# Kernel tuning notes

Hardware: AMD Instinct MI355X
Metric: run time of the kernel (lower is better)

## Reference

```python
import jax, jax.numpy as jnp
import numpy as np

B, N, D = 2, 2048, 768
HEADS, DIM_HEAD = 12, 64
INNER = HEADS * DIM_HEAD  # 768
OUT_DIM = 768


def setup_inputs() -> dict:
    key = jax.random.key(0)
    k1, k2, k3, k4, k5 = jax.random.split(key, 5)
    s_in = 1.0 / np.sqrt(D)
    s_inner = 1.0 / np.sqrt(INNER)
    return {
        "x": jax.random.normal(k1, (B, N, D), dtype=jnp.float32),
        "w_qkv": jax.random.normal(k2, (D, 3 * INNER), dtype=jnp.float32) * s_in,
        "b_qkv": jax.random.normal(k3, (3 * INNER,), dtype=jnp.float32) * 0.01,
        "w_out": jax.random.normal(k4, (INNER, OUT_DIM), dtype=jnp.float32) * s_inner,
        "b_out": jax.random.normal(k5, (OUT_DIM,), dtype=jnp.float32) * 0.01,
    }


def reference(x, w_qkv, b_qkv, w_out, b_out):
    b, n, _ = x.shape
    scale = DIM_HEAD ** -0.5
    qkv = x @ w_qkv + b_qkv                      # [b, n, 3*inner]
    q, k, v = jnp.split(qkv, 3, axis=-1)
    # 'b n (h d) -> b h n d'
    reshape = lambda t: t.reshape(b, n, HEADS, DIM_HEAD).transpose(0, 2, 1, 3)
    q, k, v = reshape(q), reshape(k), reshape(v)
    dots = jnp.einsum("bhnd,bhmd->bhnm", q, k) * scale
    attn = jax.nn.softmax(dots, axis=-1)
    out = jnp.einsum("bhnm,bhmd->bhnd", attn, v)  # [b, h, n, d]
    out = out.transpose(0, 2, 1, 3).reshape(b, n, INNER)
    return out @ w_out + b_out
```

## Files before the change

kernel.cpp:

```cpp
#include <hip/hip_runtime.h>
#include <hip/hip_bf16.h>
#include <stdint.h>


typedef __attribute__((ext_vector_type(8))) short bf16x8;
typedef __attribute__((ext_vector_type(4))) float f32x4;
typedef __attribute__((address_space(3))) unsigned int lds_uint;
typedef __attribute__((address_space(1))) const unsigned int g_uint;

__device__ __forceinline__ short f2bf(float f) {
    union { float f; uint32_t u; } x; x.f = f;
    uint32_t r = (x.u + 0x7fffu + ((x.u >> 16) & 1u)) >> 16;
    return (short)r;
}
__device__ __forceinline__ float exp2fast(float x) {
#if __has_builtin(__builtin_amdgcn_exp2f)
    return __builtin_amdgcn_exp2f(x);
#else
    return __expf(x * 0.6931471805599453f);
#endif
}
__device__ __forceinline__ void gl_lds16(const void* g, void* l) {
    __builtin_amdgcn_global_load_lds((g_uint*)g, (lds_uint*)l, 16, 0, 0);
}

__device__ __forceinline__ void tr_tile(const float* __restrict__ W,
                                        short* __restrict__ Wt, int K, int N,
                                        int n0, int k0, int t, short* S) {
    {
        int kl = t >> 2, ng = t & 3;
        const float* src = W + (size_t)(k0 + kl) * N + n0 + ng * 16;
        #pragma unroll
        for (int j = 0; j < 16; j += 4) {
            float4 f = *(const float4*)(src + j);
            S[(ng*16 + j + 0) * 65 + kl] = f2bf(f.x);
            S[(ng*16 + j + 1) * 65 + kl] = f2bf(f.y);
            S[(ng*16 + j + 2) * 65 + kl] = f2bf(f.z);
            S[(ng*16 + j + 3) * 65 + kl] = f2bf(f.w);
        }
    }
    __syncthreads();
    {
        int nl = t >> 2, kg = t & 3;
        short* dst = Wt + (size_t)(n0 + nl) * K + k0 + kg * 16;
        #pragma unroll
        for (int j = 0; j < 16; j += 4) {
            short4 s4;
            s4.x = S[nl*65 + kg*16 + j + 0];
            s4.y = S[nl*65 + kg*16 + j + 1];
            s4.z = S[nl*65 + kg*16 + j + 2];
            s4.w = S[nl*65 + kg*16 + j + 3];
            *(short4*)(dst + j) = s4;
        }
    }
}

__global__ __launch_bounds__(256)
void prep_k(const float* __restrict__ x, short* __restrict__ Xb,
            const float* __restrict__ Wq, short* __restrict__ Wqt,
            const float* __restrict__ Wo, short* __restrict__ Wot)
{
    __shared__ short S[64 * 65];
    const int t = threadIdx.x;
    if (blockIdx.x < 1536) {
        int i = (blockIdx.x * 256 + t) * 8;
        float4 f0 = *(const float4*)(x + i);
        float4 f1 = *(const float4*)(x + i + 4);
        short s[8];
        s[0]=f2bf(f0.x); s[1]=f2bf(f0.y); s[2]=f2bf(f0.z); s[3]=f2bf(f0.w);
        s[4]=f2bf(f1.x); s[5]=f2bf(f1.y); s[6]=f2bf(f1.z); s[7]=f2bf(f1.w);
        *(uint4*)(Xb + i) = *(uint4*)s;
        return;
    }
    if (blockIdx.x < 1968) {
        const int b2 = blockIdx.x - 1536;
        tr_tile(Wq, Wqt, 768, 2304, (b2 % 36) * 64, (b2 / 36) * 64, t, S);
    } else {
        const int b3 = blockIdx.x - 1968;
        tr_tile(Wo, Wot, 768, 768, (b3 % 12) * 64, (b3 / 12) * 64, t, S);
    }
}

__global__ __launch_bounds__(256)
void tr_w(const float* __restrict__ W, short* __restrict__ Wt, int K, int N) {
    __shared__ short S[64 * 65];
    tr_tile(W, Wt, K, N, blockIdx.x * 64, blockIdx.y * 64, threadIdx.x, S);
}

__global__ __launch_bounds__(256)
void gemm_qkv(const short* __restrict__ A, const short* __restrict__ Bt,
              const float* __restrict__ bias,
              short* __restrict__ Qb, short* __restrict__ Kb, short* __restrict__ Vt)
{
    __shared__ short As[128 * 32];
    __shared__ short Bs[128 * 32];
    const int tid = threadIdx.x, lane = tid & 63, w = tid >> 6;
    const int wm = w >> 1, wn = w & 1, quad = lane >> 4, lcol = lane & 15;
    const int bm = blockIdx.y * 128, bn = blockIdx.x * 128;

    f32x4 acc[4][4];
    #pragma unroll
    for (int i = 0; i < 4; i++)
        #pragma unroll
        for (int j = 0; j < 4; j++) acc[i][j] = (f32x4){0.f, 0.f, 0.f, 0.f};

    for (int kt = 0; kt < 768; kt += 32) {
        #pragma unroll
        for (int i = 0; i < 2; i++) {
            int c = tid + i * 256, row = c >> 2, cs = c & 3;
            gl_lds16(A  + (size_t)(bm + row) * 768 + kt + cs * 8, As + c * 8);
        }
        #pragma unroll
        for (int i = 0; i < 2; i++) {
            int c = tid + i * 256, row = c >> 2, cs = c & 3;
            gl_lds16(Bt + (size_t)(bn + row) * 768 + kt + cs * 8, Bs + c * 8);
        }
        __syncthreads();
        bf16x8 a[4], b[4];
        #pragma unroll
        for (int tm = 0; tm < 4; tm++)
            a[tm] = *(const bf16x8*)(As + (wm*64 + tm*16 + lcol) * 32 + quad * 8);
        #pragma unroll
        for (int tn = 0; tn < 4; tn++)
            b[tn] = *(const bf16x8*)(Bs + (wn*64 + tn*16 + lcol) * 32 + quad * 8);
        #pragma unroll
        for (int tm = 0; tm < 4; tm++)
            #pragma unroll
            for (int tn = 0; tn < 4; tn++)
                acc[tm][tn] = __builtin_amdgcn_mfma_f32_16x16x32_bf16(a[tm], b[tn], acc[tm][tn], 0, 0, 0);
        __syncthreads();
    }

    const float SCLQ = 0.18033688011112042f;
    #pragma unroll
    for (int tm = 0; tm < 4; tm++) {
        #pragma unroll
        for (int tn = 0; tn < 4; tn++) {
            int col = bn + wn*64 + tn*16 + lcol;
            float bv = bias[col];
            int which = (col >= 1536) ? 2 : (col >= 768 ? 1 : 0);
            int cc = col - which * 768;
            int h = cc >> 6, d = cc & 63;
            int rowbase = bm + wm*64 + tm*16 + quad*4;
            int bb = rowbase >> 11, n0 = rowbase & 2047;
            int bh = bb * 12 + h;
            if (which == 2) {
                short4 s4;
                s4.x = f2bf(acc[tm][tn][0] + bv);
                s4.y = f2bf(acc[tm][tn][1] + bv);
                s4.z = f2bf(acc[tm][tn][2] + bv);
                s4.w = f2bf(acc[tm][tn][3] + bv);
                *(short4*)(Vt + (((size_t)bh*32 + (n0 >> 6))*64 + d)*64 + (n0 & 63)) = s4;
            } else {
                #pragma unroll
                for (int reg = 0; reg < 4; reg++) {
                    float v = acc[tm][tn][reg] + bv;
                    if (which == 0) v *= SCLQ;
                    short* dst = (which == 0) ? Qb : Kb;
                    dst[((size_t)bh*2048 + n0 + reg)*64 + d] = f2bf(v);
                }
            }
        }
    }
}

__global__ __launch_bounds__(256)
void attn_k(const short* __restrict__ Q, const short* __restrict__ K,
            const short* __restrict__ Vt, short* __restrict__ Ab)
{
    __shared__ short Ks[2][4096];
    __shared__ short Vs[2][4096];
    __shared__ short Ps[4][16 * 72];

    const int tid = threadIdx.x, lane = tid & 63, w = tid >> 6;
    const int quad = lane >> 4, lcol = lane & 15;
    const int bid = blockIdx.x;
    const int bh = bid % 24, qt = bid / 24;
    const int b = bh / 12, h = bh - b * 12;

    const short* Kg = K  + (size_t)bh * 131072;
    const short* Vg = Vt + (size_t)bh * 131072;

    bf16x8 qf[2];
    {
        const short* Qg = Q + ((size_t)bh * 2048 + (size_t)qt * 64 + w * 16 + lcol) * 64;
        qf[0] = *(const bf16x8*)(Qg + quad * 8);
        qf[1] = *(const bf16x8*)(Qg + 32 + quad * 8);
    }

    #pragma unroll
    for (int i = 0; i < 2; i++) {
        int c = tid + i * 256, row = c >> 3, cs = c & 7, gc = cs ^ (row & 7);
        gl_lds16(Kg + row * 64 + gc * 8, Ks[0] + c * 8);
        gl_lds16(Vg + row * 64 + gc * 8, Vs[0] + c * 8);
    }
    __syncthreads();

    f32x4 o[4];
    #pragma unroll
    for (int tn = 0; tn < 4; tn++) o[tn] = (f32x4){0.f, 0.f, 0.f, 0.f};
    float lp[4] = {0.f, 0.f, 0.f, 0.f};

    short* Pw = Ps[w];

    for (int kt = 0; kt < 32; kt++) {
        const int p = kt & 1;
        if (kt < 31) {
            #pragma unroll
            for (int i = 0; i < 2; i++) {
                int c = tid + i * 256, row = c >> 3, cs = c & 7, gc = cs ^ (row & 7);
                gl_lds16(Kg + (kt + 1) * 4096 + row * 64 + gc * 8, Ks[p ^ 1] + c * 8);
                gl_lds16(Vg + (kt + 1) * 4096 + row * 64 + gc * 8, Vs[p ^ 1] + c * 8);
            }
        }

        f32x4 st[4];
        #pragma unroll
        for (int tn = 0; tn < 4; tn++) st[tn] = (f32x4){0.f, 0.f, 0.f, 0.f};
        #pragma unroll
        for (int ks = 0; ks < 2; ks++) {
            #pragma unroll
            for (int tn = 0; tn < 4; tn++) {
                int row = tn * 16 + lcol;
                bf16x8 bk = *(const bf16x8*)(Ks[p] + row * 64 +
                                             (((ks * 4 + quad) ^ (row & 7)) << 3));
                st[tn] = __builtin_amdgcn_mfma_f32_16x16x32_bf16(qf[ks], bk, st[tn], 0, 0, 0);
            }
        }

        #pragma unroll
        for (int tn = 0; tn < 4; tn++) {
            #pragma unroll
            for (int r = 0; r < 4; r++) {
                float pv = exp2fast(st[tn][r]);
                lp[r] += pv;
                union { float f; uint32_t u; } c; c.f = pv;
                Pw[(quad*4 + r) * 72 + tn*16 + lcol] = (short)((c.u + 0x8000u) >> 16);
            }
        }

        #pragma unroll
        for (int ks = 0; ks < 2; ks++) {
            bf16x8 ap = *(const bf16x8*)(Pw + lcol * 72 + ks * 32 + quad * 8);
            #pragma unroll
            for (int tn = 0; tn < 4; tn++) {
                int row = tn * 16 + lcol;
                bf16x8 bv = *(const bf16x8*)(Vs[p] + row * 64 +
                                             (((ks * 4 + quad) ^ (row & 7)) << 3));
                o[tn] = __builtin_amdgcn_mfma_f32_16x16x32_bf16(ap, bv, o[tn], 0, 0, 0);
            }
        }
        __syncthreads();
    }

    float rl[4];
    #pragma unroll
    for (int r = 0; r < 4; r++) {
        float v = lp[r];
        v += __shfl_xor(v, 1, 16);
        v += __shfl_xor(v, 2, 16);
        v += __shfl_xor(v, 4, 16);
        v += __shfl_xor(v, 8, 16);
        rl[r] = 1.0f / v;
    }
    #pragma unroll
    for (int tn = 0; tn < 4; tn++) {
        #pragma unroll
        for (int r = 0; r < 4; r++) {
            int q = qt * 64 + w * 16 + quad * 4 + r;
            int d = h * 64 + tn * 16 + lcol;
            Ab[((size_t)(b * 2048 + q)) * 768 + d] = f2bf(o[tn][r] * rl[r]);
        }
    }
}

__global__ __launch_bounds__(256)
void gemm_out64(const short* __restrict__ A, const short* __restrict__ Bt,
                const float* __restrict__ bias, float* __restrict__ Of)
{
    __shared__ short As[64 * 32];
    __shared__ short Bs[64 * 32];
    const int tid = threadIdx.x, lane = tid & 63, w = tid >> 6;
    const int wm = w >> 1, wn = w & 1, quad = lane >> 4, lcol = lane & 15;
    const int bm = blockIdx.y * 64, bn = blockIdx.x * 64;

    f32x4 acc[2][2];
    #pragma unroll
    for (int i = 0; i < 2; i++)
        #pragma unroll
        for (int j = 0; j < 2; j++) acc[i][j] = (f32x4){0.f, 0.f, 0.f, 0.f};

    for (int kt = 0; kt < 768; kt += 32) {
        {
            int row = tid >> 2, cs = tid & 3;
            gl_lds16(A  + (size_t)(bm + row) * 768 + kt + cs * 8, As + tid * 8);
            gl_lds16(Bt + (size_t)(bn + row) * 768 + kt + cs * 8, Bs + tid * 8);
        }
        __syncthreads();
        bf16x8 a[2], b[2];
        #pragma unroll
        for (int tm = 0; tm < 2; tm++)
            a[tm] = *(const bf16x8*)(As + (wm*32 + tm*16 + lcol) * 32 + quad * 8);
        #pragma unroll
        for (int tn = 0; tn < 2; tn++)
            b[tn] = *(const bf16x8*)(Bs + (wn*32 + tn*16 + lcol) * 32 + quad * 8);
        #pragma unroll
        for (int tm = 0; tm < 2; tm++)
            #pragma unroll
            for (int tn = 0; tn < 2; tn++)
                acc[tm][tn] = __builtin_amdgcn_mfma_f32_16x16x32_bf16(a[tm], b[tn], acc[tm][tn], 0, 0, 0);
        __syncthreads();
    }
    #pragma unroll
    for (int tm = 0; tm < 2; tm++) {
        #pragma unroll
        for (int tn = 0; tn < 2; tn++) {
            int col = bn + wn*32 + tn*16 + lcol;
            float bv = bias[col];
            #pragma unroll
            for (int reg = 0; reg < 4; reg++) {
                int row = bm + wm*32 + tm*16 + quad*4 + reg;
                Of[(size_t)row * 768 + col] = acc[tm][tn][reg] + bv;
            }
        }
    }
}

extern "C" void kernel_launch(void* const* d_in, const int* in_sizes, int n_in,
                              void* d_out, int out_size, void* d_ws, size_t ws_size,
                              hipStream_t stream)
{
    (void)in_sizes; (void)n_in; (void)out_size;
    const float* x     = (const float*)d_in[0];
    const float* w_qkv = (const float*)d_in[1];
    const float* b_qkv = (const float*)d_in[2];
    const float* w_out = (const float*)d_in[3];
    const float* b_out = (const float*)d_in[4];
    float* out = (float*)d_out;

    const size_t XSZ = (size_t)4096 * 768;
    const size_t WQ  = (size_t)2304 * 768;
    const size_t WO  = (size_t)768 * 768;
    const size_t HSZ = (size_t)24 * 2048 * 64;
    short* Xb  = (short*)d_ws;
    short* Wqt = Xb + XSZ;
    short* Qb  = Wqt + WQ;
    short* Kb  = Qb + HSZ;
    short* Vt  = Kb + HSZ;
    short* Ab  = Xb;

    const bool sepWot = ws_size >= (XSZ + WQ + 3*HSZ + WO) * sizeof(short);
    short* Wot = sepWot ? (Vt + HSZ) : Wqt;

    if (sepWot) {
        prep_k<<<2112, 256, 0, stream>>>(x, Xb, w_qkv, Wqt, w_out, Wot);
        gemm_qkv<<<dim3(18, 32), 256, 0, stream>>>(Xb, Wqt, b_qkv, Qb, Kb, Vt);
    } else {
        prep_k<<<1968, 256, 0, stream>>>(x, Xb, w_qkv, Wqt, w_out, Wot);
        gemm_qkv<<<dim3(18, 32), 256, 0, stream>>>(Xb, Wqt, b_qkv, Qb, Kb, Vt);
        tr_w<<<dim3(12, 12), 256, 0, stream>>>(w_out, Wot, 768, 768);
    }
    attn_k<<<768, 256, 0, stream>>>(Qb, Kb, Vt, Ab);
    gemm_out64<<<dim3(12, 64), 256, 0, stream>>>(Ab, Wot, b_out, out);
}
```

Measured before the change: 181.5 us.

## Enlarge attention query tile to 128 rows and widen output GEMM tile

The attention kernel now runs 512 threads per block covering 128 query rows, so each K/V tile load to LDS is shared by twice as many queries. Each thread now issues one async load per tile instead of two. Bf16 packing of the probabilities uses the paired conversion intrinsic, and the P buffer row stride changes from 72 to 68. The output projection GEMM widens its N tile to 96 with a 2x3 MFMA layout per warp, which improves operand reuse. The cost is fewer blocks (384 attention, 512 GEMM), which lowers parallelism on a large-CU device, and possible LDS bank conflicts from the new stride.

Measured after the change: 203.4 us. 1.12x slower.

```diff
diff --git a/kernel.cpp b/kernel.cpp
--- a/kernel.cpp
+++ b/kernel.cpp
@@ -164,13 +164,13 @@
     }
 }
 
-__global__ __launch_bounds__(256)
+__global__ __launch_bounds__(512)
 void attn_k(const short* __restrict__ Q, const short* __restrict__ K,
             const short* __restrict__ Vt, short* __restrict__ Ab)
 {
     __shared__ short Ks[2][4096];
     __shared__ short Vs[2][4096];
-    __shared__ short Ps[4][16 * 72];
+    __shared__ short Ps[8][16 * 68];
 
     const int tid = threadIdx.x, lane = tid & 63, w = tid >> 6;
     const int quad = lane >> 4, lcol = lane & 15;
@@ -183,14 +183,13 @@
 
     bf16x8 qf[2];
     {
-        const short* Qg = Q + ((size_t)bh * 2048 + (size_t)qt * 64 + w * 16 + lcol) * 64;
+        const short* Qg = Q + ((size_t)bh * 2048 + (size_t)qt * 128 + w * 16 + lcol) * 64;
         qf[0] = *(const bf16x8*)(Qg + quad * 8);
         qf[1] = *(const bf16x8*)(Qg + 32 + quad * 8);
     }
 
-    #pragma unroll
-    for (int i = 0; i < 2; i++) {
-        int c = tid + i * 256, row = c >> 3, cs = c & 7, gc = cs ^ (row & 7);
+    {
+        int c = tid, row = c >> 3, cs = c & 7, gc = cs ^ (row & 7);
         gl_lds16(Kg + row * 64 + gc * 8, Ks[0] + c * 8);
         gl_lds16(Vg + row * 64 + gc * 8, Vs[0] + c * 8);
     }
@@ -206,12 +205,9 @@
     for (int kt = 0; kt < 32; kt++) {
         const int p = kt & 1;
         if (kt < 31) {
-            #pragma unroll
-            for (int i = 0; i < 2; i++) {
-                int c = tid + i * 256, row = c >> 3, cs = c & 7, gc = cs ^ (row & 7);
-                gl_lds16(Kg + (kt + 1) * 4096 + row * 64 + gc * 8, Ks[p ^ 1] + c * 8);
-                gl_lds16(Vg + (kt + 1) * 4096 + row * 64 + gc * 8, Vs[p ^ 1] + c * 8);
-            }
+            int c = tid, row = c >> 3, cs = c & 7, gc = cs ^ (row & 7);
+            gl_lds16(Kg + (kt + 1) * 4096 + row * 64 + gc * 8, Ks[p ^ 1] + c * 8);
+            gl_lds16(Vg + (kt + 1) * 4096 + row * 64 + gc * 8, Vs[p ^ 1] + c * 8);
         }
 
         f32x4 st[4];
@@ -230,18 +226,21 @@
 
         #pragma unroll
         for (int tn = 0; tn < 4; tn++) {
-            #pragma unroll
-            for (int r = 0; r < 4; r++) {
-                float pv = exp2fast(st[tn][r]);
-                lp[r] += pv;
-                union { float f; uint32_t u; } c; c.f = pv;
-                Pw[(quad*4 + r) * 72 + tn*16 + lcol] = (short)((c.u + 0x8000u) >> 16);
-            }
+            float p0 = exp2fast(st[tn][0]), p1 = exp2fast(st[tn][1]);
+            float p2 = exp2fast(st[tn][2]), p3 = exp2fast(st[tn][3]);
+            lp[0] += p0; lp[1] += p1; lp[2] += p2; lp[3] += p3;
+            union { __hip_bfloat162 h2; uint32_t u; short s[2]; } c01, c23;
+            c01.h2 = __float22bfloat162_rn(make_float2(p0, p1));
+            c23.h2 = __float22bfloat162_rn(make_float2(p2, p3));
+            Pw[(quad*4 + 0) * 68 + tn*16 + lcol] = c01.s[0];
+            Pw[(quad*4 + 1) * 68 + tn*16 + lcol] = c01.s[1];
+            Pw[(quad*4 + 2) * 68 + tn*16 + lcol] = c23.s[0];
+            Pw[(quad*4 + 3) * 68 + tn*16 + lcol] = c23.s[1];
         }
 
         #pragma unroll
         for (int ks = 0; ks < 2; ks++) {
-            bf16x8 ap = *(const bf16x8*)(Pw + lcol * 72 + ks * 32 + quad * 8);
+            bf16x8 ap = *(const bf16x8*)(Pw + lcol * 68 + ks * 32 + quad * 8);
             #pragma unroll
             for (int tn = 0; tn < 4; tn++) {
                 int row = tn * 16 + lcol;
@@ -267,7 +266,7 @@
     for (int tn = 0; tn < 4; tn++) {
         #pragma unroll
         for (int r = 0; r < 4; r++) {
-            int q = qt * 64 + w * 16 + quad * 4 + r;
+            int q = qt * 128 + w * 16 + quad * 4 + r;
             int d = h * 64 + tn * 16 + lcol;
             Ab[((size_t)(b * 2048 + q)) * 768 + d] = f2bf(o[tn][r] * rl[r]);
         }
@@ -275,20 +274,20 @@
 }
 
 __global__ __launch_bounds__(256)
-void gemm_out64(const short* __restrict__ A, const short* __restrict__ Bt,
-                const float* __restrict__ bias, float* __restrict__ Of)
+void gemm_out(const short* __restrict__ A, const short* __restrict__ Bt,
+              const float* __restrict__ bias, float* __restrict__ Of)
 {
     __shared__ short As[64 * 32];
-    __shared__ short Bs[64 * 32];
+    __shared__ short Bs[96 * 32];
     const int tid = threadIdx.x, lane = tid & 63, w = tid >> 6;
     const int wm = w >> 1, wn = w & 1, quad = lane >> 4, lcol = lane & 15;
-    const int bm = blockIdx.y * 64, bn = blockIdx.x * 64;
-
-    f32x4 acc[2][2];
+    const int bm = blockIdx.y * 64, bn = blockIdx.x * 96;
+
+    f32x4 acc[2][3];
     #pragma unroll
     for (int i = 0; i < 2; i++)
         #pragma unroll
-        for (int j = 0; j < 2; j++) acc[i][j] = (f32x4){0.f, 0.f, 0.f, 0.f};
+        for (int j = 0; j < 3; j++) acc[i][j] = (f32x4){0.f, 0.f, 0.f, 0.f};
 
     for (int kt = 0; kt < 768; kt += 32) {
         {
@@ -296,26 +295,30 @@
             gl_lds16(A  + (size_t)(bm + row) * 768 + kt + cs * 8, As + tid * 8);
             gl_lds16(Bt + (size_t)(bn + row) * 768 + kt + cs * 8, Bs + tid * 8);
         }
-        __syncthreads();
-        bf16x8 a[2], b[2];
+        if (tid < 128) {
+            int c = 256 + tid, row = c >> 2, cs = c & 3;
+            gl_lds16(Bt + (size_t)(bn + row) * 768 + kt + cs * 8, Bs + c * 8);
+        }
+        __syncthreads();
+        bf16x8 a[2], b[3];
         #pragma unroll
         for (int tm = 0; tm < 2; tm++)
             a[tm] = *(const bf16x8*)(As + (wm*32 + tm*16 + lcol) * 32 + quad * 8);
         #pragma unroll
-        for (int tn = 0; tn < 2; tn++)
-            b[tn] = *(const bf16x8*)(Bs + (wn*32 + tn*16 + lcol) * 32 + quad * 8);
+        for (int tn = 0; tn < 3; tn++)
+            b[tn] = *(const bf16x8*)(Bs + (wn*48 + tn*16 + lcol) * 32 + quad * 8);
         #pragma unroll
         for (int tm = 0; tm < 2; tm++)
             #pragma unroll
-            for (int tn = 0; tn < 2; tn++)
+            for (int tn = 0; tn < 3; tn++)
                 acc[tm][tn] = __builtin_amdgcn_mfma_f32_16x16x32_bf16(a[tm], b[tn], acc[tm][tn], 0, 0, 0);
         __syncthreads();
     }
     #pragma unroll
     for (int tm = 0; tm < 2; tm++) {
         #pragma unroll
-        for (int tn = 0; tn < 2; tn++) {
-            int col = bn + wn*32 + tn*16 + lcol;
+        for (int tn = 0; tn < 3; tn++) {
+            int col = bn + wn*48 + tn*16 + lcol;
             float bv = bias[col];
             #pragma unroll
             for (int reg = 0; reg < 4; reg++) {
@@ -360,6 +363,6 @@
         gemm_qkv<<<dim3(18, 32), 256, 0, stream>>>(Xb, Wqt, b_qkv, Qb, Kb, Vt);
         tr_w<<<dim3(12, 12), 256, 0, stream>>>(w_out, Wot, 768, 768);
     }
-    attn_k<<<768, 256, 0, stream>>>(Qb, Kb, Vt, Ab);
-    gemm_out64<<<dim3(12, 64), 256, 0, stream>>>(Ab, Wot, b_out, out);
-}
+    attn_k<<<384, 512, 0, stream>>>(Qb, Kb, Vt, Ab);
+    gemm_out<<<dim3(8, 64), 256, 0, stream>>>(Ab, Wot, b_out, out);
+}
```
